# Optimization experiments

Measured on AMD Instinct MI355X. Metric: run time of the kernel, lower is better.

The kernel has to match this reference:

```python
import jax, jax.numpy as jnp
import numpy as np

N_NODES = 10000
N_EDGES = 200000
F = 128
NB = 20
LN_EPS = 1e-5

act = jax.nn.silu

def mlp2(x, W1, b1, W2, b2):
    # two-layer MLP: Linear -> silu -> Linear (weights stored [in, out])
    h = act(jnp.dot(x, W1) + b1)
    return jnp.dot(h, W2) + b2

def mlp2_nobias(x, W1, W2):
    return jnp.dot(act(jnp.dot(x, W1)), W2)

def layernorm(x, g, b):
    mu = jnp.mean(x, axis=-1, keepdims=True)
    var = jnp.mean(jnp.square(x - mu), axis=-1, keepdims=True)
    return (x - mu) * jax.lax.rsqrt(var + LN_EPS) * g + b

def setup_inputs() -> dict:
    key = jax.random.key(0)
    ks = jax.random.split(key, 32)
    s = 1.0 / np.sqrt(F)
    d = {
        "atom_node": jax.random.normal(ks[0], (N_NODES, F), jnp.float32),
        "force_node": jax.random.normal(ks[1], (N_NODES, 3, F), jnp.float32),
        "disp_node": jax.random.normal(ks[2], (N_NODES, 3, F), jnp.float32),
        "disp_edge": jax.random.normal(ks[3], (N_EDGES, 3), jnp.float32),
        "dist_edge": jax.random.uniform(ks[4], (N_EDGES, NB), jnp.float32),
        "edge_index": jax.random.randint(ks[5], (2, N_EDGES), 0, N_NODES, jnp.int32),
        # inv_message_nodepart
        "nmp_W1": jax.random.normal(ks[6], (F, F), jnp.float32) * s,
        "nmp_b1": jnp.zeros((F,), jnp.float32),
        "nmp_W2": jax.random.normal(ks[7], (F, F), jnp.float32) * s,
        "nmp_b2": jnp.zeros((F,), jnp.float32),
        # inv_message_edgepart
        "emp_W": jax.random.normal(ks[8], (NB, F), jnp.float32) * (1.0 / np.sqrt(NB)),
        "emp_b": jnp.zeros((F,), jnp.float32),
        # equiv_message1
        "eq1_W1": jax.random.normal(ks[9], (F, F), jnp.float32) * s,
        "eq1_b1": jnp.zeros((F,), jnp.float32),
        "eq1_W2": jax.random.normal(ks[10], (F, F), jnp.float32) * s,
        "eq1_b2": jnp.zeros((F,), jnp.float32),
        # equiv_message2
        "eq2_W1": jax.random.normal(ks[11], (F, F), jnp.float32) * s,
        "eq2_b1": jnp.zeros((F,), jnp.float32),
        "eq2_W2": jax.random.normal(ks[12], (F, F), jnp.float32) * s,
        "eq2_b2": jnp.zeros((F,), jnp.float32),
        # equiv_message3 (no bias)
        "eq3_W1": jax.random.normal(ks[13], (F, F), jnp.float32) * s,
        "eq3_W2": jax.random.normal(ks[14], (F, F), jnp.float32) * s,
        # inv_update
        "upd_W1": jax.random.normal(ks[15], (F, F), jnp.float32) * s,
        "upd_b1": jnp.zeros((F,), jnp.float32),
        "upd_W2": jax.random.normal(ks[16], (F, F), jnp.float32) * s,
        "upd_b2": jnp.zeros((F,), jnp.float32),
        # LayerNorm
        "ln_g": jnp.ones((F,), jnp.float32),
        "ln_b": jnp.zeros((F,), jnp.float32),
    }
    return d

def reference(atom_node, force_node, disp_node, disp_edge, dist_edge, edge_index,
              nmp_W1, nmp_b1, nmp_W2, nmp_b2, emp_W, emp_b,
              eq1_W1, eq1_b1, eq1_W2, eq1_b2,
              eq2_W1, eq2_b1, eq2_W2, eq2_b2,
              eq3_W1, eq3_W2,
              upd_W1, upd_b1, upd_W2, upd_b2,
              ln_g, ln_b):
    n = atom_node.shape[0]
    src = edge_index[0]
    dst = edge_index[1]
    seg = lambda x: jax.ops.segment_sum(x, src, num_segments=n)

    # invariant message: edge part * node parts gathered at both endpoints
    h = mlp2(atom_node, nmp_W1, nmp_b1, nmp_W2, nmp_b2)            # [N, F]
    e = jnp.dot(dist_edge, emp_W) + emp_b                           # [E, F]
    inv_message = e * h[src] * h[dst]                               # [E, F]
    atom_node = atom_node + seg(inv_message)

    # equivariant message 1: radial MLP * displacement vectors
    eq1 = mlp2(inv_message, eq1_W1, eq1_b1, eq1_W2, eq1_b2)[:, None, :] \
          * disp_edge[:, :, None]                                   # [E, 3, F]
    agg1 = seg(eq1)                                                 # [N, 3, F]
    force_node = force_node + agg1

    # equivariant message 2: edge MLP * neighbor displacement features (pre-update)
    eq2 = mlp2(inv_message, eq2_W1, eq2_b1, eq2_W2, eq2_b2)[:, None, :] \
          * disp_node[dst]                                          # [E, 3, F]
    disp_node = disp_node + seg(eq2)

    # equivariant message 3: scatter-then-gather of agg1 with invariant gate
    eq3_inv = mlp2_nobias(atom_node, eq3_W1, eq3_W2)                # [N, F]
    eq3 = eq3_inv[dst][:, None, :] * agg1[dst]                      # [E, 3, F]
    disp_node = disp_node + seg(eq3)

    # invariant update coupling force and displacement channels
    inv_update = mlp2(atom_node, upd_W1, upd_b1, upd_W2, upd_b2) \
                 * jnp.sum(-force_node * disp_node, axis=-2)        # [N, F]
    atom_node = layernorm(atom_node + inv_update, ln_g, ln_b)
    return (atom_node, force_node, disp_node)
```

## Files before the change

### kernel.cpp

```cpp
#include <hip/hip_runtime.h>
#include <hip/hip_bf16.h>

#define F 128
#define NB 20
#define KP 32
#define HSTRIDE 136

typedef __attribute__((ext_vector_type(8))) short short8;
typedef __attribute__((ext_vector_type(4))) short short4v;
typedef __attribute__((ext_vector_type(4))) float floatx4;

__device__ __forceinline__ float silu_f(float x) {
    return x * __builtin_amdgcn_rcpf(1.0f + __expf(-x));
}
__device__ __forceinline__ float bfs2f(short s) {
    unsigned int u = ((unsigned int)(unsigned short)s) << 16;
    float f; __builtin_memcpy(&f, &u, 4); return f;
}

__device__ __forceinline__ void stage_issue(const __hip_bfloat16* W, int t,
                                            short8 wreg[4]) {
#pragma unroll
    for (int r = 0; r < 4; ++r)
        wreg[r] = *(const short8*)(W + (size_t)(r * 512 + t) * 8);
}
__device__ __forceinline__ void stage_write(__hip_bfloat16* wbuf, int t,
                                            const short8 wreg[4]) {
#pragma unroll
    for (int r = 0; r < 4; ++r) {
        const int c = r * 512 + t;
        *(short8*)(wbuf + (size_t)(c >> 4) * HSTRIDE + (c & 15) * 8) = wreg[r];
    }
}

template<typename OUT_T, bool BIAS>
__global__ __launch_bounds__(256) void fused_mlp_kernel(
    const __hip_bfloat16* __restrict__ X,
    const __hip_bfloat16* __restrict__ Wt1, const float* __restrict__ b1,
    const __hip_bfloat16* __restrict__ Wt2, const float* __restrict__ b2,
    OUT_T* __restrict__ Y, int Mp)
{
    __shared__ __hip_bfloat16 hid[128 * HSTRIDE];
    const int t = threadIdx.x;
    const int wave = t >> 6;
    const int lane = t & 63;
    const int quad = lane >> 4;
    const int l16  = lane & 15;
    const int eloc0 = wave * 32;
    const int e0 = blockIdx.x * 128 + eloc0;

    floatx4 acc[8][2];
#pragma unroll
    for (int ft = 0; ft < 8; ++ft)
#pragma unroll
        for (int et = 0; et < 2; ++et)
            acc[ft][et] = (floatx4){0.f, 0.f, 0.f, 0.f};

#pragma unroll
    for (int ks = 0; ks < 4; ++ks) {
        const int k0 = ks * 32 + quad * 8;
        short8 bx[2], aw[8];
#pragma unroll
        for (int et = 0; et < 2; ++et)
            bx[et] = *(const short8*)(X + (size_t)(e0 + et * 16 + l16) * F + k0);
#pragma unroll
        for (int ft = 0; ft < 8; ++ft)
            aw[ft] = *(const short8*)(Wt1 + (size_t)(ft * 16 + l16) * F + k0);
#pragma unroll
        for (int ft = 0; ft < 8; ++ft)
#pragma unroll
            for (int et = 0; et < 2; ++et)
                acc[ft][et] = __builtin_amdgcn_mfma_f32_16x16x32_bf16(
                    aw[ft], bx[et], acc[ft][et], 0, 0, 0);
    }

#pragma unroll
    for (int ft = 0; ft < 8; ++ft) {
        const int feat = ft * 16 + quad * 4;
        floatx4 bv = (floatx4){0.f, 0.f, 0.f, 0.f};
        if (BIAS) bv = *(const floatx4*)(b1 + feat);
#pragma unroll
        for (int et = 0; et < 2; ++et) {
            const int el = eloc0 + et * 16 + l16;
            __align__(8) __hip_bfloat16 tmp[4];
#pragma unroll
            for (int r = 0; r < 4; ++r)
                tmp[r] = __float2bfloat16(silu_f(acc[ft][et][r] + bv[r]));
            *(short4v*)(hid + (size_t)el * HSTRIDE + feat) = *(const short4v*)tmp;
        }
    }
    __builtin_amdgcn_sched_barrier(0);

#pragma unroll
    for (int ft = 0; ft < 8; ++ft)
#pragma unroll
        for (int et = 0; et < 2; ++et)
            acc[ft][et] = (floatx4){0.f, 0.f, 0.f, 0.f};

#pragma unroll
    for (int ks = 0; ks < 4; ++ks) {
        const int k0 = ks * 32 + quad * 8;
        short8 bx[2], aw[8];
#pragma unroll
        for (int et = 0; et < 2; ++et)
            bx[et] = *(const short8*)(hid + (size_t)(eloc0 + et * 16 + l16) * HSTRIDE + k0);
#pragma unroll
        for (int ft = 0; ft < 8; ++ft)
            aw[ft] = *(const short8*)(Wt2 + (size_t)(ft * 16 + l16) * F + k0);
#pragma unroll
        for (int ft = 0; ft < 8; ++ft)
#pragma unroll
            for (int et = 0; et < 2; ++et)
                acc[ft][et] = __builtin_amdgcn_mfma_f32_16x16x32_bf16(
                    aw[ft], bx[et], acc[ft][et], 0, 0, 0);
    }

#pragma unroll
    for (int ft = 0; ft < 8; ++ft) {
        const int feat = ft * 16 + quad * 4;
        floatx4 bv = (floatx4){0.f, 0.f, 0.f, 0.f};
        if (BIAS) bv = *(const floatx4*)(b2 + feat);
#pragma unroll
        for (int et = 0; et < 2; ++et) {
            const int e = e0 + et * 16 + l16;
            if (sizeof(OUT_T) == 2) {
                __align__(8) __hip_bfloat16 tmp[4];
#pragma unroll
                for (int r = 0; r < 4; ++r)
                    tmp[r] = __float2bfloat16(acc[ft][et][r] + bv[r]);
                *(short4v*)((__hip_bfloat16*)Y + (size_t)e * F + feat) = *(const short4v*)tmp;
            } else {
                floatx4 v;
#pragma unroll
                for (int r = 0; r < 4; ++r) v[r] = acc[ft][et][r] + bv[r];
                *(floatx4*)((float*)Y + (size_t)e * F + feat) = v;
            }
        }
    }
}

template<typename OUTA, typename OUTB, bool BIASA, bool BIASB>
__global__ __launch_bounds__(512, 4) void dual_mlp_kernel(
    const __hip_bfloat16* X,
    const __hip_bfloat16* __restrict__ W1a, const float* __restrict__ b1a,
    const __hip_bfloat16* __restrict__ W2a, const float* __restrict__ b2a,
    const __hip_bfloat16* __restrict__ W1b, const float* __restrict__ b1b,
    const __hip_bfloat16* __restrict__ W2b, const float* __restrict__ b2b,
    OUTA* __restrict__ Q1, OUTB* Q2, int Mp)
{
    __shared__ __hip_bfloat16 hid[128 * HSTRIDE];
    __shared__ __hip_bfloat16 wbuf[128 * HSTRIDE];
    const int t = threadIdx.x;
    const int wave = t >> 6;
    const int rg   = wave >> 1;
    const int wf   = wave & 1;
    const int lane = t & 63;
    const int quad = lane >> 4;
    const int l16  = lane & 15;
    const int eloc0 = rg * 32;
    const int e0 = blockIdx.x * 128 + eloc0;
    const int fbase = wf * 64;

    short8 bxk[4][2];
#pragma unroll
    for (int ks = 0; ks < 4; ++ks)
#pragma unroll
        for (int et = 0; et < 2; ++et)
            bxk[ks][et] = *(const short8*)(X + (size_t)(e0 + et * 16 + l16) * F
                                           + ks * 32 + quad * 8);

    short8 wreg[4];
    floatx4 acc[4][2];

    stage_issue(W1a, t, wreg);
    stage_write(wbuf, t, wreg);
    __syncthreads();

    stage_issue(W2a, t, wreg);
    __builtin_amdgcn_sched_barrier(0);
#pragma unroll
    for (int ft = 0; ft < 4; ++ft)
#pragma unroll
        for (int et = 0; et < 2; ++et)
            acc[ft][et] = (floatx4){0.f, 0.f, 0.f, 0.f};
#pragma unroll
    for (int ks = 0; ks < 4; ++ks) {
        const int k0 = ks * 32 + quad * 8;
        short8 aw[4];
#pragma unroll
        for (int ft = 0; ft < 4; ++ft)
            aw[ft] = *(const short8*)(wbuf + (size_t)(fbase + ft * 16 + l16) * HSTRIDE + k0);
#pragma unroll
        for (int ft = 0; ft < 4; ++ft)
#pragma unroll
            for (int et = 0; et < 2; ++et)
                acc[ft][et] = __builtin_amdgcn_mfma_f32_16x16x32_bf16(
                    aw[ft], bxk[ks][et], acc[ft][et], 0, 0, 0);
    }
#pragma unroll
    for (int ft = 0; ft < 4; ++ft) {
        const int feat = fbase + ft * 16 + quad * 4;
        floatx4 bv = (floatx4){0.f, 0.f, 0.f, 0.f};
        if (BIASA) bv = *(const floatx4*)(b1a + feat);
#pragma unroll
        for (int et = 0; et < 2; ++et) {
            const int el = eloc0 + et * 16 + l16;
            __align__(8) __hip_bfloat16 tmp[4];
#pragma unroll
            for (int r = 0; r < 4; ++r)
                tmp[r] = __float2bfloat16(silu_f(acc[ft][et][r] + bv[r]));
            *(short4v*)(hid + (size_t)el * HSTRIDE + feat) = *(const short4v*)tmp;
        }
    }
    __syncthreads();
    stage_write(wbuf, t, wreg);
    __syncthreads();

    stage_issue(W1b, t, wreg);
    __builtin_amdgcn_sched_barrier(0);
#pragma unroll
    for (int ft = 0; ft < 4; ++ft)
#pragma unroll
        for (int et = 0; et < 2; ++et)
            acc[ft][et] = (floatx4){0.f, 0.f, 0.f, 0.f};
#pragma unroll
    for (int ks = 0; ks < 4; ++ks) {
        const int k0 = ks * 32 + quad * 8;
        short8 bh[2], aw[4];
#pragma unroll
        for (int et = 0; et < 2; ++et)
            bh[et] = *(const short8*)(hid + (size_t)(eloc0 + et * 16 + l16) * HSTRIDE + k0);
#pragma unroll
        for (int ft = 0; ft < 4; ++ft)
            aw[ft] = *(const short8*)(wbuf + (size_t)(fbase + ft * 16 + l16) * HSTRIDE + k0);
#pragma unroll
        for (int ft = 0; ft < 4; ++ft)
#pragma unroll
            for (int et = 0; et < 2; ++et)
                acc[ft][et] = __builtin_amdgcn_mfma_f32_16x16x32_bf16(
                    aw[ft], bh[et], acc[ft][et], 0, 0, 0);
    }
#pragma unroll
    for (int ft = 0; ft < 4; ++ft) {
        const int feat = fbase + ft * 16 + quad * 4;
        floatx4 bv = (floatx4){0.f, 0.f, 0.f, 0.f};
        if (BIASA) bv = *(const floatx4*)(b2a + feat);
#pragma unroll
        for (int et = 0; et < 2; ++et) {
            const int e = e0 + et * 16 + l16;
            if (sizeof(OUTA) == 2) {
                __align__(8) __hip_bfloat16 tmp[4];
#pragma unroll
                for (int r = 0; r < 4; ++r)
                    tmp[r] = __float2bfloat16(acc[ft][et][r] + bv[r]);
                *(short4v*)((__hip_bfloat16*)Q1 + (size_t)e * F + feat) = *(const short4v*)tmp;
            } else {
                floatx4 v;
#pragma unroll
                for (int r = 0; r < 4; ++r) v[r] = acc[ft][et][r] + bv[r];
                *(floatx4*)((float*)Q1 + (size_t)e * F + feat) = v;
            }
        }
    }
    __syncthreads();
    stage_write(wbuf, t, wreg);
    __syncthreads();

    stage_issue(W2b, t, wreg);
    __builtin_amdgcn_sched_barrier(0);
#pragma unroll
    for (int ft = 0; ft < 4; ++ft)
#pragma unroll
        for (int et = 0; et < 2; ++et)
            acc[ft][et] = (floatx4){0.f, 0.f, 0.f, 0.f};
#pragma unroll
    for (int ks = 0; ks < 4; ++ks) {
        const int k0 = ks * 32 + quad * 8;
        short8 aw[4];
#pragma unroll
        for (int ft = 0; ft < 4; ++ft)
            aw[ft] = *(const short8*)(wbuf + (size_t)(fbase + ft * 16 + l16) * HSTRIDE + k0);
#pragma unroll
        for (int ft = 0; ft < 4; ++ft)
#pragma unroll
            for (int et = 0; et < 2; ++et)
                acc[ft][et] = __builtin_amdgcn_mfma_f32_16x16x32_bf16(
                    aw[ft], bxk[ks][et], acc[ft][et], 0, 0, 0);
    }
#pragma unroll
    for (int ft = 0; ft < 4; ++ft) {
        const int feat = fbase + ft * 16 + quad * 4;
        floatx4 bv = (floatx4){0.f, 0.f, 0.f, 0.f};
        if (BIASB) bv = *(const floatx4*)(b1b + feat);
#pragma unroll
        for (int et = 0; et < 2; ++et) {
            const int el = eloc0 + et * 16 + l16;
            __align__(8) __hip_bfloat16 tmp[4];
#pragma unroll
            for (int r = 0; r < 4; ++r)
                tmp[r] = __float2bfloat16(silu_f(acc[ft][et][r] + bv[r]));
            *(short4v*)(hid + (size_t)el * HSTRIDE + feat) = *(const short4v*)tmp;
        }
    }
    __syncthreads();
    stage_write(wbuf, t, wreg);
    __syncthreads();

#pragma unroll
    for (int ft = 0; ft < 4; ++ft)
#pragma unroll
        for (int et = 0; et < 2; ++et)
            acc[ft][et] = (floatx4){0.f, 0.f, 0.f, 0.f};
#pragma unroll
    for (int ks = 0; ks < 4; ++ks) {
        const int k0 = ks * 32 + quad * 8;
        short8 bh[2], aw[4];
#pragma unroll
        for (int et = 0; et < 2; ++et)
            bh[et] = *(const short8*)(hid + (size_t)(eloc0 + et * 16 + l16) * HSTRIDE + k0);
#pragma unroll
        for (int ft = 0; ft < 4; ++ft)
            aw[ft] = *(const short8*)(wbuf + (size_t)(fbase + ft * 16 + l16) * HSTRIDE + k0);
#pragma unroll
        for (int ft = 0; ft < 4; ++ft)
#pragma unroll
            for (int et = 0; et < 2; ++et)
                acc[ft][et] = __builtin_amdgcn_mfma_f32_16x16x32_bf16(
                    aw[ft], bh[et], acc[ft][et], 0, 0, 0);
    }
#pragma unroll
    for (int ft = 0; ft < 4; ++ft) {
        const int feat = fbase + ft * 16 + quad * 4;
        floatx4 bv = (floatx4){0.f, 0.f, 0.f, 0.f};
        if (BIASB) bv = *(const floatx4*)(b2b + feat);
#pragma unroll
        for (int et = 0; et < 2; ++et) {
            const int e = e0 + et * 16 + l16;
            if (sizeof(OUTB) == 2) {
                __align__(8) __hip_bfloat16 tmp[4];
#pragma unroll
                for (int r = 0; r < 4; ++r)
                    tmp[r] = __float2bfloat16(acc[ft][et][r] + bv[r]);
                *(short4v*)((__hip_bfloat16*)Q2 + (size_t)e * F + feat) = *(const short4v*)tmp;
            } else {
                floatx4 v;
#pragma unroll
                for (int r = 0; r < 4; ++r) v[r] = acc[ft][et][r] + bv[r];
                *(floatx4*)((float*)Q2 + (size_t)e * F + feat) = v;
            }
        }
    }
}

__global__ __launch_bounds__(256) void edge_inv_mfma_kernel(
    const __hip_bfloat16* __restrict__ dist_p,
    const __hip_bfloat16* __restrict__ empWt,
    const float* __restrict__ emp_b, const __hip_bfloat16* __restrict__ h,
    const int* __restrict__ src_p, const int* __restrict__ dst_p,
    __hip_bfloat16* __restrict__ Xbf, int E)
{
    const int t = threadIdx.x;
    const int wave = t >> 6;
    const int lane = t & 63;
    const int quad = lane >> 4;
    const int l16  = lane & 15;
    const int e0 = blockIdx.x * 128 + wave * 32;

    short8 bx[2], aw[8];
#pragma unroll
    for (int et = 0; et < 2; ++et)
        bx[et] = *(const short8*)(dist_p + (size_t)(e0 + et * 16 + l16) * KP + quad * 8);
#pragma unroll
    for (int ft = 0; ft < 8; ++ft)
        aw[ft] = *(const short8*)(empWt + (size_t)(ft * 16 + l16) * KP + quad * 8);

    floatx4 acc[8][2];
#pragma unroll
    for (int ft = 0; ft < 8; ++ft)
#pragma unroll
        for (int et = 0; et < 2; ++et)
            acc[ft][et] = __builtin_amdgcn_mfma_f32_16x16x32_bf16(
                aw[ft], bx[et], (floatx4){0.f, 0.f, 0.f, 0.f}, 0, 0, 0);

    int eidx[2], sR[2], dR[2];
#pragma unroll
    for (int et = 0; et < 2; ++et) {
        eidx[et] = e0 + et * 16 + l16;
        const bool v = eidx[et] < E;
        sR[et] = v ? src_p[eidx[et]] : 0;
        dR[et] = v ? dst_p[eidx[et]] : 0;
    }

#pragma unroll
    for (int ft = 0; ft < 8; ++ft) {
        const int feat = ft * 16 + quad * 4;
        const floatx4 bv = *(const floatx4*)(emp_b + feat);
#pragma unroll
        for (int et = 0; et < 2; ++et) {
            const short4v hs = *(const short4v*)(h + (size_t)sR[et] * F + feat);
            const short4v hd = *(const short4v*)(h + (size_t)dR[et] * F + feat);
            const bool v = eidx[et] < E;
            __align__(8) __hip_bfloat16 tmp[4];
#pragma unroll
            for (int r = 0; r < 4; ++r) {
                const float m = v ? (acc[ft][et][r] + bv[r]) * bfs2f(hs[r]) * bfs2f(hd[r])
                                  : 0.0f;
                tmp[r] = __float2bfloat16(m);
            }
            *(short4v*)(Xbf + (size_t)eidx[et] * F + feat) = *(const short4v*)tmp;
        }
    }
}


__global__ void prep_weights_kernel(
    const float* __restrict__ W0, const float* __restrict__ W1,
    const float* __restrict__ W2, const float* __restrict__ W3,
    const float* __restrict__ W4, const float* __restrict__ W5,
    const float* __restrict__ W6, const float* __restrict__ W7,
    const float* __restrict__ W8, const float* __restrict__ W9,
    __hip_bfloat16* __restrict__ Wt)
{
    const int t = blockIdx.x * 256 + threadIdx.x;
    if (t >= 10 * F * F) return;
    const int w = t >> 14;
    const int idx = t & (F * F - 1);
    const int n = idx >> 7;
    const int k = idx & 127;
    const float* W = (w == 0) ? W0 : (w == 1) ? W1 : (w == 2) ? W2 : (w == 3) ? W3
                   : (w == 4) ? W4 : (w == 5) ? W5 : (w == 6) ? W6 : (w == 7) ? W7
                   : (w == 8) ? W8 : W9;
    Wt[t] = __float2bfloat16(W[k * F + n]);
}

__global__ void prep_empw_kernel(const float* __restrict__ emp_W,
                                 __hip_bfloat16* __restrict__ empWt)
{
    const int t = blockIdx.x * 256 + threadIdx.x;
    if (t >= F * KP) return;
    const int n = t >> 5;
    const int k = t & (KP - 1);
    empWt[t] = __float2bfloat16(k < NB ? emp_W[k * F + n] : 0.0f);
}

__global__ void cast_pad_kernel(const float* __restrict__ src,
                                __hip_bfloat16* __restrict__ dst,
                                int n_valid, int n_total)
{
    const int stride = gridDim.x * blockDim.x;
    for (int i = blockIdx.x * blockDim.x + threadIdx.x; i < n_total; i += stride)
        dst[i] = __float2bfloat16(i < n_valid ? src[i] : 0.0f);
}

__global__ void pad_zero_bf_kernel(__hip_bfloat16* __restrict__ dst,
                                   int from, int to)
{
    const int i = from + blockIdx.x * 256 + threadIdx.x;
    if (i < to) dst[i] = __float2bfloat16(0.0f);
}


__global__ void zero_counts_kernel(int* __restrict__ counts, int N) {
    const int stride = gridDim.x * blockDim.x;
    for (int i = blockIdx.x * blockDim.x + threadIdx.x; i < N; i += stride)
        counts[i] = 0;
}

__global__ void csr_count_kernel(const int* __restrict__ src,
                                 int* __restrict__ counts, int E) {
    const int stride = gridDim.x * blockDim.x;
    for (int e = blockIdx.x * blockDim.x + threadIdx.x; e < E; e += stride)
        atomicAdd(&counts[src[e]], 1);
}

__global__ __launch_bounds__(1024) void csr_scan_kernel(
    const int* __restrict__ counts, int* __restrict__ offsets,
    int* __restrict__ cursor, int N)
{
    constexpr int T = 1024;
    const int t = threadIdx.x;
    const int per = (N + T - 1) / T;
    const int base = t * per;
    int lsum = 0;
    for (int i = 0; i < per; ++i) {
        int idx = base + i;
        if (idx < N) lsum += counts[idx];
    }
    __shared__ int s[T];
    s[t] = lsum;
    __syncthreads();
    for (int off = 1; off < T; off <<= 1) {
        int v = (t >= off) ? s[t - off] : 0;
        __syncthreads();
        s[t] += v;
        __syncthreads();
    }
    int run = s[t] - lsum;
    for (int i = 0; i < per; ++i) {
        int idx = base + i;
        if (idx < N) {
            offsets[idx] = run;
            cursor[idx] = run;
            run += counts[idx];
        }
    }
    if (t == T - 1) offsets[N] = run;
}

__global__ void csr_perm_kernel(const int* __restrict__ src,
                                const int* __restrict__ dst,
                                const float* __restrict__ disp_edge,
                                const float* __restrict__ dist_edge,
                                int* __restrict__ cursor,
                                int* __restrict__ src_p,
                                int* __restrict__ dst_p,
                                float* __restrict__ de_p,
                                __hip_bfloat16* __restrict__ dist_p, int E) {
    const int stride = gridDim.x * blockDim.x;
    for (int e = blockIdx.x * blockDim.x + threadIdx.x; e < E; e += stride) {
        const int s = src[e];
        const int pos = atomicAdd(&cursor[s], 1);
        src_p[pos] = s;
        dst_p[pos] = dst[e];
        de_p[3 * pos + 0] = disp_edge[3 * e + 0];
        de_p[3 * pos + 1] = disp_edge[3 * e + 1];
        de_p[3 * pos + 2] = disp_edge[3 * e + 2];
        __align__(16) __hip_bfloat16 tmp[KP];
#pragma unroll
        for (int k = 0; k < KP; ++k)
            tmp[k] = __float2bfloat16(k < NB ? dist_edge[(size_t)e * NB + k] : 0.0f);
#pragma unroll
        for (int q = 0; q < 4; ++q)
            *(short8*)(dist_p + (size_t)pos * KP + q * 8) = ((const short8*)tmp)[q];
    }
}


__global__ __launch_bounds__(128) void gather_inv_kernel(
    const __hip_bfloat16* __restrict__ inv_msg, const int* __restrict__ offsets,
    const float* __restrict__ atom,
    float* __restrict__ atom_new, __hip_bfloat16* __restrict__ atom_new_bf, int N)
{
    const int n = blockIdx.x;
    if (n >= N) return;
    const int j = threadIdx.x;
    const int p1 = offsets[n + 1];
    float acc = 0.0f;
    for (int p = offsets[n]; p < p1; ++p)
        acc += __bfloat162float(inv_msg[(size_t)p * F + j]);
    const float v = atom[(size_t)n * F + j] + acc;
    atom_new[(size_t)n * F + j] = v;
    atom_new_bf[(size_t)n * F + j] = __float2bfloat16(v);
}

__global__ __launch_bounds__(128) void gather_eq1_kernel(
    const __hip_bfloat16* __restrict__ eqm, const float* __restrict__ de_p,
    const int* __restrict__ offsets,
    const float* __restrict__ force, const float* __restrict__ disp_node,
    const __hip_bfloat16* __restrict__ eq3i_bf,
    float* __restrict__ out_force, ushort2* __restrict__ pk, int N)
{
    const int n = blockIdx.x;
    if (n >= N) return;
    const int j = threadIdx.x;
    const int p1 = offsets[n + 1];
    float a0 = 0.0f, a1 = 0.0f, a2 = 0.0f;
    for (int p = offsets[n]; p < p1; ++p) {
        const float m = __bfloat162float(eqm[(size_t)p * F + j]);
        a0 = fmaf(m, de_p[(size_t)p * 3 + 0], a0);
        a1 = fmaf(m, de_p[(size_t)p * 3 + 1], a1);
        a2 = fmaf(m, de_p[(size_t)p * 3 + 2], a2);
    }
    const float g = __bfloat162float(eq3i_bf[(size_t)n * F + j]);
    const size_t b = (size_t)n * 3 * F + j;
    out_force[b]         = force[b] + a0;
    out_force[b + F]     = force[b + F] + a1;
    out_force[b + 2 * F] = force[b + 2 * F] + a2;
    __hip_bfloat16 d0 = __float2bfloat16(disp_node[b]);
    __hip_bfloat16 d1 = __float2bfloat16(disp_node[b + F]);
    __hip_bfloat16 d2 = __float2bfloat16(disp_node[b + 2 * F]);
    __hip_bfloat16 v0 = __float2bfloat16(g * a0);
    __hip_bfloat16 v1 = __float2bfloat16(g * a1);
    __hip_bfloat16 v2 = __float2bfloat16(g * a2);
    pk[b]         = make_ushort2(*(unsigned short*)&d0, *(unsigned short*)&v0);
    pk[b + F]     = make_ushort2(*(unsigned short*)&d1, *(unsigned short*)&v1);
    pk[b + 2 * F] = make_ushort2(*(unsigned short*)&d2, *(unsigned short*)&v2);
}

__global__ __launch_bounds__(128) void gather_eq23_kernel(
    const __hip_bfloat16* __restrict__ eqm2, const ushort2* __restrict__ pk,
    const float* __restrict__ disp_node,
    const int* __restrict__ dst_p, const int* __restrict__ offsets,
    float* __restrict__ out_disp, int N)
{
    const int n = blockIdx.x;
    if (n >= N) return;
    const int j = threadIdx.x;
    const int p1 = offsets[n + 1];
    float a0 = 0.0f, a1 = 0.0f, a2 = 0.0f;
    for (int p = offsets[n]; p < p1; ++p) {
        const int d = dst_p[p];
        const float m = __bfloat162float(eqm2[(size_t)p * F + j]);
        const ushort2 c0 = pk[(size_t)d * 3 * F + j];
        const ushort2 c1 = pk[(size_t)d * 3 * F + F + j];
        const ushort2 c2 = pk[(size_t)d * 3 * F + 2 * F + j];
        a0 += m * bfs2f((short)c0.x) + bfs2f((short)c0.y);
        a1 += m * bfs2f((short)c1.x) + bfs2f((short)c1.y);
        a2 += m * bfs2f((short)c2.x) + bfs2f((short)c2.y);
    }
    const size_t b = (size_t)n * 3 * F + j;
    out_disp[b]         = disp_node[b] + a0;
    out_disp[b + F]     = disp_node[b + F] + a1;
    out_disp[b + 2 * F] = disp_node[b + 2 * F] + a2;
}


__global__ __launch_bounds__(128) void update_ln_kernel(
    const float* __restrict__ atom_new, const float* __restrict__ upd,
    const float* __restrict__ out_force, const float* __restrict__ out_disp,
    const float* __restrict__ ln_g, const float* __restrict__ ln_b,
    float* __restrict__ out_atom, int N)
{
    const int n = blockIdx.x;
    if (n >= N) return;
    const int j = threadIdx.x;
    __shared__ float red[4];

    const float* fo = out_force + (size_t)n * (3 * F) + j;
    const float* dl = out_disp + (size_t)n * (3 * F) + j;
    const float s = -(fo[0] * dl[0] + fo[F] * dl[F] + fo[2 * F] * dl[2 * F]);
    const float y = atom_new[(size_t)n * F + j] + upd[(size_t)n * F + j] * s;

    float sy = y, syy = y * y;
#pragma unroll
    for (int m = 1; m < 64; m <<= 1) {
        sy  += __shfl_xor(sy, m);
        syy += __shfl_xor(syy, m);
    }
    if ((j & 63) == 0) {
        red[(j >> 6) * 2 + 0] = sy;
        red[(j >> 6) * 2 + 1] = syy;
    }
    __syncthreads();
    const float tsy  = red[0] + red[2];
    const float tsyy = red[1] + red[3];
    const float mu = tsy * (1.0f / F);
    float var = tsyy * (1.0f / F) - mu * mu;
    if (var < 0.0f) var = 0.0f;
    const float rstd = rsqrtf(var + 1e-5f);
    out_atom[(size_t)n * F + j] = (y - mu) * rstd * ln_g[j] + ln_b[j];
}

extern "C" void kernel_launch(void* const* d_in, const int* in_sizes, int n_in,
                              void* d_out, int out_size, void* d_ws, size_t ws_size,
                              hipStream_t stream)
{
    const float* atom_node  = (const float*)d_in[0];
    const float* force_node = (const float*)d_in[1];
    const float* disp_node  = (const float*)d_in[2];
    const float* disp_edge  = (const float*)d_in[3];
    const float* dist_edge  = (const float*)d_in[4];
    const int*   edge_index = (const int*)d_in[5];
    const float* nmp_W1 = (const float*)d_in[6];
    const float* nmp_b1 = (const float*)d_in[7];
    const float* nmp_W2 = (const float*)d_in[8];
    const float* nmp_b2 = (const float*)d_in[9];
    const float* emp_W  = (const float*)d_in[10];
    const float* emp_b  = (const float*)d_in[11];
    const float* eq1_W1 = (const float*)d_in[12];
    const float* eq1_b1 = (const float*)d_in[13];
    const float* eq1_W2 = (const float*)d_in[14];
    const float* eq1_b2 = (const float*)d_in[15];
    const float* eq2_W1 = (const float*)d_in[16];
    const float* eq2_b1 = (const float*)d_in[17];
    const float* eq2_W2 = (const float*)d_in[18];
    const float* eq2_b2 = (const float*)d_in[19];
    const float* eq3_W1 = (const float*)d_in[20];
    const float* eq3_W2 = (const float*)d_in[21];
    const float* upd_W1 = (const float*)d_in[22];
    const float* upd_b1 = (const float*)d_in[23];
    const float* upd_W2 = (const float*)d_in[24];
    const float* upd_b2 = (const float*)d_in[25];
    const float* ln_g   = (const float*)d_in[26];
    const float* ln_b   = (const float*)d_in[27];

    const int N = in_sizes[0] / F;
    const int E = in_sizes[4] / NB;
    const int Mp  = ((E + 127) / 128) * 128;
    const int Mp2 = ((N + 127) / 128) * 128;
    const int* src = edge_index;
    const int* dst = edge_index + E;
    const int nF = N * F, n3F = N * 3 * F;

    float* out_atom  = (float*)d_out;
    float* out_force = out_atom + (size_t)nF;
    float* out_disp  = out_force + (size_t)n3F;

    char* p = (char*)d_ws;
    int* counts  = (int*)p;
    int* offsets = counts + N;
    int* cursor  = offsets + (N + 1);
    int* src_p   = cursor + N;
    int* dst_p   = src_p + E;
    size_t off = (size_t)(3 * N + 1 + 2 * E) * sizeof(int);
    off = (off + 63) & ~(size_t)63;
    float* de_p = (float*)(p + off); off += (size_t)3 * E * sizeof(float);
    off = (off + 63) & ~(size_t)63;
    __hip_bfloat16* dist_p = (__hip_bfloat16*)(p + off); off += (size_t)Mp * KP * 2;
    __hip_bfloat16* empWt  = (__hip_bfloat16*)(p + off); off += (size_t)F * KP * 2;

    __hip_bfloat16* h_bf        = (__hip_bfloat16*)(p + off); off += (size_t)Mp2 * F * 2;
    __hip_bfloat16* atom_bf     = (__hip_bfloat16*)(p + off); off += (size_t)Mp2 * F * 2;
    __hip_bfloat16* atom_new_bf = (__hip_bfloat16*)(p + off); off += (size_t)Mp2 * F * 2;
    __hip_bfloat16* eq3i_bf     = (__hip_bfloat16*)(p + off); off += (size_t)Mp2 * F * 2;
    off = (off + 63) & ~(size_t)63;
    float* atom_new = (float*)(p + off); off += (size_t)nF * 4;
    float* upd_f    = (float*)(p + off); off += (size_t)Mp2 * F * 4;
    ushort2* pk     = (ushort2*)(p + off); off += (size_t)n3F * sizeof(ushort2);
    off = (off + 63) & ~(size_t)63;
    __hip_bfloat16* Xbf = (__hip_bfloat16*)(p + off); off += (size_t)Mp * F * 2;
    __hip_bfloat16* Q1  = (__hip_bfloat16*)(p + off); off += (size_t)Mp * F * 2;
    __hip_bfloat16* Q2  = Xbf;
    __hip_bfloat16* Wt  = (__hip_bfloat16*)(p + off);
    __hip_bfloat16* Wt_eq1a = Wt + 0 * F * F;
    __hip_bfloat16* Wt_eq1b = Wt + 1 * F * F;
    __hip_bfloat16* Wt_eq2a = Wt + 2 * F * F;
    __hip_bfloat16* Wt_eq2b = Wt + 3 * F * F;
    __hip_bfloat16* Wt_nmpa = Wt + 4 * F * F;
    __hip_bfloat16* Wt_nmpb = Wt + 5 * F * F;
    __hip_bfloat16* Wt_eq3a = Wt + 6 * F * F;
    __hip_bfloat16* Wt_eq3b = Wt + 7 * F * F;
    __hip_bfloat16* Wt_upda = Wt + 8 * F * F;
    __hip_bfloat16* Wt_updb = Wt + 9 * F * F;

    prep_weights_kernel<<<(10 * F * F + 255) / 256, 256, 0, stream>>>(
        eq1_W1, eq1_W2, eq2_W1, eq2_W2, nmp_W1, nmp_W2, eq3_W1, eq3_W2,
        upd_W1, upd_W2, Wt);
    prep_empw_kernel<<<(F * KP + 255) / 256, 256, 0, stream>>>(emp_W, empWt);
    cast_pad_kernel<<<512, 256, 0, stream>>>(atom_node, atom_bf, nF, Mp2 * F);
    pad_zero_bf_kernel<<<(Mp2 * F - nF + 255) / 256, 256, 0, stream>>>(
        atom_new_bf, nF, Mp2 * F);
    zero_counts_kernel<<<64, 256, 0, stream>>>(counts, N);
    csr_count_kernel<<<256, 256, 0, stream>>>(src, counts, E);
    csr_scan_kernel<<<1, 1024, 0, stream>>>(counts, offsets, cursor, N);
    csr_perm_kernel<<<256, 256, 0, stream>>>(src, dst, disp_edge, dist_edge,
                                             cursor, src_p, dst_p, de_p, dist_p, E);

    fused_mlp_kernel<__hip_bfloat16, true><<<Mp2 / 128, 256, 0, stream>>>(
        atom_bf, Wt_nmpa, nmp_b1, Wt_nmpb, nmp_b2, h_bf, Mp2);

    edge_inv_mfma_kernel<<<Mp / 128, 256, 0, stream>>>(
        dist_p, empWt, emp_b, h_bf, src_p, dst_p, Xbf, E);
    gather_inv_kernel<<<N, 128, 0, stream>>>(Xbf, offsets, atom_node,
                                             atom_new, atom_new_bf, N);

    dual_mlp_kernel<__hip_bfloat16, float, false, true><<<Mp2 / 128, 512, 0, stream>>>(
        atom_new_bf, Wt_eq3a, nullptr, Wt_eq3b, nullptr,
        Wt_upda, upd_b1, Wt_updb, upd_b2, eq3i_bf, upd_f, Mp2);

    dual_mlp_kernel<__hip_bfloat16, __hip_bfloat16, true, true>
        <<<Mp / 128, 512, 0, stream>>>(
        Xbf, Wt_eq1a, eq1_b1, Wt_eq1b, eq1_b2,
        Wt_eq2a, eq2_b1, Wt_eq2b, eq2_b2, Q1, Q2, Mp);

    gather_eq1_kernel<<<N, 128, 0, stream>>>(Q1, de_p, offsets, force_node,
                                             disp_node, eq3i_bf, out_force, pk, N);
    gather_eq23_kernel<<<N, 128, 0, stream>>>(Q2, pk, disp_node, dst_p,
                                              offsets, out_disp, N);

    update_ln_kernel<<<N, 128, 0, stream>>>(atom_new, upd_f, out_force, out_disp,
                                            ln_g, ln_b, out_atom, N);
}
```

Measured before the change: 456.2 us.

## Map one wave per node in gathers and stage edge node rows in LDS

The four per-node gather/update kernels now assign one 64-lane wave per node with two features per lane. Four nodes share a 256-thread block, and loads and stores are vectorized. In the layernorm kernel this lets the block-level shared-memory reduction and barrier become a pure wave shuffle reduction. The edge invariant kernel first cooperatively loads the source and destination h rows for its 128 edges into a padded LDS buffer, overlapping these gathers with the MFMA work. The gather_eq23 loop also prefetches the next dst index. The costs are about 70KB of LDS per edge block, which lowers occupancy, plus extra barriers.

New measurement: 442.4 us. 1.03x faster.

```diff
diff --git a/kernel.cpp b/kernel.cpp
--- a/kernel.cpp
+++ b/kernel.cpp
@@ -5,6 +5,7 @@
 #define NB 20
 #define KP 32
 #define HSTRIDE 136
+#define HROWS_STRIDE 140
 
 typedef __attribute__((ext_vector_type(8))) short short8;
 typedef __attribute__((ext_vector_type(4))) short short4v;
@@ -16,6 +17,13 @@
 __device__ __forceinline__ float bfs2f(short s) {
     unsigned int u = ((unsigned int)(unsigned short)s) << 16;
     float f; __builtin_memcpy(&f, &u, 4); return f;
+}
+__device__ __forceinline__ float lo_bf(unsigned int u) { return bfs2f((short)(u & 0xFFFF)); }
+__device__ __forceinline__ float hi_bf(unsigned int u) { return bfs2f((short)(u >> 16)); }
+__device__ __forceinline__ unsigned int pack_bf2(float d, float v) {
+    __hip_bfloat16 db = __float2bfloat16(d), vb = __float2bfloat16(v);
+    return (unsigned int)*(unsigned short*)&db
+         | ((unsigned int)*(unsigned short*)&vb << 16);
 }
 
 __device__ __forceinline__ void stage_issue(const __hip_bfloat16* W, int t,
@@ -359,12 +367,34 @@
     const int* __restrict__ src_p, const int* __restrict__ dst_p,
     __hip_bfloat16* __restrict__ Xbf, int E)
 {
+    __shared__ __hip_bfloat16 hrows[256 * HROWS_STRIDE];
+    __shared__ int ridx[256];
     const int t = threadIdx.x;
     const int wave = t >> 6;
     const int lane = t & 63;
     const int quad = lane >> 4;
     const int l16  = lane & 15;
-    const int e0 = blockIdx.x * 128 + wave * 32;
+    const int e0b = blockIdx.x * 128;
+    const int e0 = e0b + wave * 32;
+
+    {
+        const int le = (t < 128) ? t : (t - 128);
+        const int e = e0b + le;
+        const int idx = (e < E) ? ((t < 128) ? src_p[e] : dst_p[e]) : 0;
+        ridx[t] = idx;
+    }
+    __syncthreads();
+
+#pragma unroll
+    for (int i = 0; i < 16; ++i) {
+        const int idx = i * 256 + t;
+        const int r = idx >> 4, part = idx & 15;
+        const short8 v = *(const short8*)(h + (size_t)ridx[r] * F + part * 8);
+        const short4v lo = __builtin_shufflevector(v, v, 0, 1, 2, 3);
+        const short4v hi = __builtin_shufflevector(v, v, 4, 5, 6, 7);
+        *(short4v*)(hrows + (size_t)r * HROWS_STRIDE + part * 8)     = lo;
+        *(short4v*)(hrows + (size_t)r * HROWS_STRIDE + part * 8 + 4) = hi;
+    }
 
     short8 bx[2], aw[8];
 #pragma unroll
@@ -382,14 +412,11 @@
             acc[ft][et] = __builtin_amdgcn_mfma_f32_16x16x32_bf16(
                 aw[ft], bx[et], (floatx4){0.f, 0.f, 0.f, 0.f}, 0, 0, 0);
 
-    int eidx[2], sR[2], dR[2];
-#pragma unroll
-    for (int et = 0; et < 2; ++et) {
-        eidx[et] = e0 + et * 16 + l16;
-        const bool v = eidx[et] < E;
-        sR[et] = v ? src_p[eidx[et]] : 0;
-        dR[et] = v ? dst_p[eidx[et]] : 0;
-    }
+    __syncthreads();
+
+    int eidx[2];
+#pragma unroll
+    for (int et = 0; et < 2; ++et) eidx[et] = e0 + et * 16 + l16;
 
 #pragma unroll
     for (int ft = 0; ft < 8; ++ft) {
@@ -397,8 +424,9 @@
         const floatx4 bv = *(const floatx4*)(emp_b + feat);
 #pragma unroll
         for (int et = 0; et < 2; ++et) {
-            const short4v hs = *(const short4v*)(h + (size_t)sR[et] * F + feat);
-            const short4v hd = *(const short4v*)(h + (size_t)dR[et] * F + feat);
+            const int le = wave * 32 + et * 16 + l16;
+            const short4v hs = *(const short4v*)(hrows + (size_t)le * HROWS_STRIDE + feat);
+            const short4v hd = *(const short4v*)(hrows + (size_t)(128 + le) * HROWS_STRIDE + feat);
             const bool v = eidx[et] < E;
             __align__(8) __hip_bfloat16 tmp[4];
 #pragma unroll
@@ -536,119 +564,152 @@
 }
 
 
-__global__ __launch_bounds__(128) void gather_inv_kernel(
+__global__ __launch_bounds__(256) void gather_inv_kernel(
     const __hip_bfloat16* __restrict__ inv_msg, const int* __restrict__ offsets,
     const float* __restrict__ atom,
     float* __restrict__ atom_new, __hip_bfloat16* __restrict__ atom_new_bf, int N)
 {
-    const int n = blockIdx.x;
+    const int n = blockIdx.x * 4 + (threadIdx.x >> 6);
     if (n >= N) return;
-    const int j = threadIdx.x;
-    const int p1 = offsets[n + 1];
-    float acc = 0.0f;
-    for (int p = offsets[n]; p < p1; ++p)
-        acc += __bfloat162float(inv_msg[(size_t)p * F + j]);
-    const float v = atom[(size_t)n * F + j] + acc;
-    atom_new[(size_t)n * F + j] = v;
-    atom_new_bf[(size_t)n * F + j] = __float2bfloat16(v);
-}
-
-__global__ __launch_bounds__(128) void gather_eq1_kernel(
+    const int f0 = (threadIdx.x & 63) * 2;
+    const int p0 = offsets[n], p1 = offsets[n + 1];
+    float a0 = 0.0f, a1 = 0.0f;
+    for (int p = p0; p < p1; ++p) {
+        const unsigned int u = *(const unsigned int*)(inv_msg + (size_t)p * F + f0);
+        a0 += lo_bf(u);
+        a1 += hi_bf(u);
+    }
+    const float2 av = *(const float2*)(atom + (size_t)n * F + f0);
+    const float v0 = av.x + a0, v1 = av.y + a1;
+    *(float2*)(atom_new + (size_t)n * F + f0) = make_float2(v0, v1);
+    __hip_bfloat16 b0 = __float2bfloat16(v0), b1 = __float2bfloat16(v1);
+    *(ushort2*)(atom_new_bf + (size_t)n * F + f0) =
+        make_ushort2(*(unsigned short*)&b0, *(unsigned short*)&b1);
+}
+
+__global__ __launch_bounds__(256) void gather_eq1_kernel(
     const __hip_bfloat16* __restrict__ eqm, const float* __restrict__ de_p,
     const int* __restrict__ offsets,
     const float* __restrict__ force, const float* __restrict__ disp_node,
     const __hip_bfloat16* __restrict__ eq3i_bf,
     float* __restrict__ out_force, ushort2* __restrict__ pk, int N)
 {
-    const int n = blockIdx.x;
+    const int n = blockIdx.x * 4 + (threadIdx.x >> 6);
     if (n >= N) return;
-    const int j = threadIdx.x;
-    const int p1 = offsets[n + 1];
-    float a0 = 0.0f, a1 = 0.0f, a2 = 0.0f;
-    for (int p = offsets[n]; p < p1; ++p) {
-        const float m = __bfloat162float(eqm[(size_t)p * F + j]);
-        a0 = fmaf(m, de_p[(size_t)p * 3 + 0], a0);
-        a1 = fmaf(m, de_p[(size_t)p * 3 + 1], a1);
-        a2 = fmaf(m, de_p[(size_t)p * 3 + 2], a2);
-    }
-    const float g = __bfloat162float(eq3i_bf[(size_t)n * F + j]);
-    const size_t b = (size_t)n * 3 * F + j;
-    out_force[b]         = force[b] + a0;
-    out_force[b + F]     = force[b + F] + a1;
-    out_force[b + 2 * F] = force[b + 2 * F] + a2;
-    __hip_bfloat16 d0 = __float2bfloat16(disp_node[b]);
-    __hip_bfloat16 d1 = __float2bfloat16(disp_node[b + F]);
-    __hip_bfloat16 d2 = __float2bfloat16(disp_node[b + 2 * F]);
-    __hip_bfloat16 v0 = __float2bfloat16(g * a0);
-    __hip_bfloat16 v1 = __float2bfloat16(g * a1);
-    __hip_bfloat16 v2 = __float2bfloat16(g * a2);
-    pk[b]         = make_ushort2(*(unsigned short*)&d0, *(unsigned short*)&v0);
-    pk[b + F]     = make_ushort2(*(unsigned short*)&d1, *(unsigned short*)&v1);
-    pk[b + 2 * F] = make_ushort2(*(unsigned short*)&d2, *(unsigned short*)&v2);
-}
-
-__global__ __launch_bounds__(128) void gather_eq23_kernel(
+    const int f0 = (threadIdx.x & 63) * 2;
+    const int p0 = offsets[n], p1 = offsets[n + 1];
+    float a00 = 0.f, a01 = 0.f, a10 = 0.f, a11 = 0.f, a20 = 0.f, a21 = 0.f;
+    for (int p = p0; p < p1; ++p) {
+        const unsigned int u = *(const unsigned int*)(eqm + (size_t)p * F + f0);
+        const float m0 = lo_bf(u), m1 = hi_bf(u);
+        const float d0 = de_p[(size_t)p * 3 + 0];
+        const float d1 = de_p[(size_t)p * 3 + 1];
+        const float d2 = de_p[(size_t)p * 3 + 2];
+        a00 = fmaf(m0, d0, a00); a01 = fmaf(m1, d0, a01);
+        a10 = fmaf(m0, d1, a10); a11 = fmaf(m1, d1, a11);
+        a20 = fmaf(m0, d2, a20); a21 = fmaf(m1, d2, a21);
+    }
+    const unsigned int ug = *(const unsigned int*)(eq3i_bf + (size_t)n * F + f0);
+    const float g0 = lo_bf(ug), g1 = hi_bf(ug);
+    const size_t b = (size_t)n * 3 * F + f0;
+
+    float2 f;
+    f = *(const float2*)(force + b);
+    *(float2*)(out_force + b) = make_float2(f.x + a00, f.y + a01);
+    f = *(const float2*)(force + b + F);
+    *(float2*)(out_force + b + F) = make_float2(f.x + a10, f.y + a11);
+    f = *(const float2*)(force + b + 2 * F);
+    *(float2*)(out_force + b + 2 * F) = make_float2(f.x + a20, f.y + a21);
+
+    float2 dn;
+    dn = *(const float2*)(disp_node + b);
+    *(uint2*)(pk + b) = make_uint2(pack_bf2(dn.x, g0 * a00), pack_bf2(dn.y, g1 * a01));
+    dn = *(const float2*)(disp_node + b + F);
+    *(uint2*)(pk + b + F) = make_uint2(pack_bf2(dn.x, g0 * a10), pack_bf2(dn.y, g1 * a11));
+    dn = *(const float2*)(disp_node + b + 2 * F);
+    *(uint2*)(pk + b + 2 * F) = make_uint2(pack_bf2(dn.x, g0 * a20), pack_bf2(dn.y, g1 * a21));
+}
+
+__global__ __launch_bounds__(256) void gather_eq23_kernel(
     const __hip_bfloat16* __restrict__ eqm2, const ushort2* __restrict__ pk,
     const float* __restrict__ disp_node,
     const int* __restrict__ dst_p, const int* __restrict__ offsets,
     float* __restrict__ out_disp, int N)
 {
-    const int n = blockIdx.x;
+    const int n = blockIdx.x * 4 + (threadIdx.x >> 6);
     if (n >= N) return;
-    const int j = threadIdx.x;
-    const int p1 = offsets[n + 1];
-    float a0 = 0.0f, a1 = 0.0f, a2 = 0.0f;
-    for (int p = offsets[n]; p < p1; ++p) {
-        const int d = dst_p[p];
-        const float m = __bfloat162float(eqm2[(size_t)p * F + j]);
-        const ushort2 c0 = pk[(size_t)d * 3 * F + j];
-        const ushort2 c1 = pk[(size_t)d * 3 * F + F + j];
-        const ushort2 c2 = pk[(size_t)d * 3 * F + 2 * F + j];
-        a0 += m * bfs2f((short)c0.x) + bfs2f((short)c0.y);
-        a1 += m * bfs2f((short)c1.x) + bfs2f((short)c1.y);
-        a2 += m * bfs2f((short)c2.x) + bfs2f((short)c2.y);
-    }
-    const size_t b = (size_t)n * 3 * F + j;
-    out_disp[b]         = disp_node[b] + a0;
-    out_disp[b + F]     = disp_node[b + F] + a1;
-    out_disp[b + 2 * F] = disp_node[b + 2 * F] + a2;
-}
-
-
-__global__ __launch_bounds__(128) void update_ln_kernel(
+    const int f0 = (threadIdx.x & 63) * 2;
+    const int p0 = offsets[n], p1 = offsets[n + 1];
+    float a00 = 0.f, a01 = 0.f, a10 = 0.f, a11 = 0.f, a20 = 0.f, a21 = 0.f;
+    int d = (p0 < p1) ? dst_p[p0] : 0;
+    for (int p = p0; p < p1; ++p) {
+        const int dn = (p + 1 < p1) ? dst_p[p + 1] : 0;
+        const unsigned int u = *(const unsigned int*)(eqm2 + (size_t)p * F + f0);
+        const float m0 = lo_bf(u), m1 = hi_bf(u);
+        const size_t pb = (size_t)d * 3 * F + f0;
+        const uint2 c0 = *(const uint2*)(pk + pb);
+        const uint2 c1 = *(const uint2*)(pk + pb + F);
+        const uint2 c2 = *(const uint2*)(pk + pb + 2 * F);
+        a00 += m0 * lo_bf(c0.x) + hi_bf(c0.x);
+        a01 += m1 * lo_bf(c0.y) + hi_bf(c0.y);
+        a10 += m0 * lo_bf(c1.x) + hi_bf(c1.x);
+        a11 += m1 * lo_bf(c1.y) + hi_bf(c1.y);
+        a20 += m0 * lo_bf(c2.x) + hi_bf(c2.x);
+        a21 += m1 * lo_bf(c2.y) + hi_bf(c2.y);
+        d = dn;
+    }
+    const size_t b = (size_t)n * 3 * F + f0;
+    float2 dn2;
+    dn2 = *(const float2*)(disp_node + b);
+    *(float2*)(out_disp + b) = make_float2(dn2.x + a00, dn2.y + a01);
+    dn2 = *(const float2*)(disp_node + b + F);
+    *(float2*)(out_disp + b + F) = make_float2(dn2.x + a10, dn2.y + a11);
+    dn2 = *(const float2*)(disp_node + b + 2 * F);
+    *(float2*)(out_disp + b + 2 * F) = make_float2(dn2.x + a20, dn2.y + a21);
+}
+
+
+__global__ __launch_bounds__(256) void update_ln_kernel(
     const float* __restrict__ atom_new, const float* __restrict__ upd,
     const float* __restrict__ out_force, const float* __restrict__ out_disp,
     const float* __restrict__ ln_g, const float* __restrict__ ln_b,
     float* __restrict__ out_atom, int N)
 {
-    const int n = blockIdx.x;
+    const int n = blockIdx.x * 4 + (threadIdx.x >> 6);
     if (n >= N) return;
-    const int j = threadIdx.x;
-    __shared__ float red[4];
-
-    const float* fo = out_force + (size_t)n * (3 * F) + j;
-    const float* dl = out_disp + (size_t)n * (3 * F) + j;
-    const float s = -(fo[0] * dl[0] + fo[F] * dl[F] + fo[2 * F] * dl[2 * F]);
-    const float y = atom_new[(size_t)n * F + j] + upd[(size_t)n * F + j] * s;
-
-    float sy = y, syy = y * y;
+    const int f0 = (threadIdx.x & 63) * 2;
+    const size_t b = (size_t)n * 3 * F + f0;
+
+    const float2 fo0 = *(const float2*)(out_force + b);
+    const float2 fo1 = *(const float2*)(out_force + b + F);
+    const float2 fo2 = *(const float2*)(out_force + b + 2 * F);
+    const float2 dl0 = *(const float2*)(out_disp + b);
+    const float2 dl1 = *(const float2*)(out_disp + b + F);
+    const float2 dl2 = *(const float2*)(out_disp + b + 2 * F);
+    const float s0 = -(fo0.x * dl0.x + fo1.x * dl1.x + fo2.x * dl2.x);
+    const float s1 = -(fo0.y * dl0.y + fo1.y * dl1.y + fo2.y * dl2.y);
+
+    const float2 an = *(const float2*)(atom_new + (size_t)n * F + f0);
+    const float2 up = *(const float2*)(upd + (size_t)n * F + f0);
+    const float y0 = an.x + up.x * s0;
+    const float y1 = an.y + up.y * s1;
+
+    float sy = y0 + y1, syy = y0 * y0 + y1 * y1;
 #pragma unroll
     for (int m = 1; m < 64; m <<= 1) {
         sy  += __shfl_xor(sy, m);
         syy += __shfl_xor(syy, m);
     }
-    if ((j & 63) == 0) {
-        red[(j >> 6) * 2 + 0] = sy;
-        red[(j >> 6) * 2 + 1] = syy;
-    }
-    __syncthreads();
-    const float tsy  = red[0] + red[2];
-    const float tsyy = red[1] + red[3];
-    const float mu = tsy * (1.0f / F);
-    float var = tsyy * (1.0f / F) - mu * mu;
+    const float mu = sy * (1.0f / F);
+    float var = syy * (1.0f / F) - mu * mu;
     if (var < 0.0f) var = 0.0f;
     const float rstd = rsqrtf(var + 1e-5f);
-    out_atom[(size_t)n * F + j] = (y - mu) * rstd * ln_g[j] + ln_b[j];
+
+    const float2 gg = *(const float2*)(ln_g + f0);
+    const float2 bb = *(const float2*)(ln_b + f0);
+    *(float2*)(out_atom + (size_t)n * F + f0) =
+        make_float2((y0 - mu) * rstd * gg.x + bb.x,
+                    (y1 - mu) * rstd * gg.y + bb.y);
 }
 
 extern "C" void kernel_launch(void* const* d_in, const int* in_sizes, int n_in,
@@ -751,8 +812,8 @@
 
     edge_inv_mfma_kernel<<<Mp / 128, 256, 0, stream>>>(
         dist_p, empWt, emp_b, h_bf, src_p, dst_p, Xbf, E);
-    gather_inv_kernel<<<N, 128, 0, stream>>>(Xbf, offsets, atom_node,
-                                             atom_new, atom_new_bf, N);
+    gather_inv_kernel<<<(N + 3) / 4, 256, 0, stream>>>(Xbf, offsets, atom_node,
+                                                       atom_new, atom_new_bf, N);
 
     dual_mlp_kernel<__hip_bfloat16, float, false, true><<<Mp2 / 128, 512, 0, stream>>>(
         atom_new_bf, Wt_eq3a, nullptr, Wt_eq3b, nullptr,
@@ -763,11 +824,11 @@
         Xbf, Wt_eq1a, eq1_b1, Wt_eq1b, eq1_b2,
         Wt_eq2a, eq2_b1, Wt_eq2b, eq2_b2, Q1, Q2, Mp);
 
-    gather_eq1_kernel<<<N, 128, 0, stream>>>(Q1, de_p, offsets, force_node,
-                                             disp_node, eq3i_bf, out_force, pk, N);
-    gather_eq23_kernel<<<N, 128, 0, stream>>>(Q2, pk, disp_node, dst_p,
-                                              offsets, out_disp, N);
-
-    update_ln_kernel<<<N, 128, 0, stream>>>(atom_new, upd_f, out_force, out_disp,
-                                            ln_g, ln_b, out_atom, N);
-}
+    gather_eq1_kernel<<<(N + 3) / 4, 256, 0, stream>>>(
+        Q1, de_p, offsets, force_node, disp_node, eq3i_bf, out_force, pk, N);
+    gather_eq23_kernel<<<(N + 3) / 4, 256, 0, stream>>>(
+        Q2, pk, disp_node, dst_p, offsets, out_disp, N);
+
+    update_ln_kernel<<<(N + 3) / 4, 256, 0, stream>>>(
+        atom_new, upd_f, out_force, out_disp, ln_g, ln_b, out_atom, N);
+}
```
